# Performance work log

Hardware: AMD Instinct MI355X
Metric: run time of the kernel (lower is better)

## Reference

```python
import jax, jax.numpy as jnp
import numpy as np

B, C, H, W = 32, 2, 224, 224
P = 4096   # mask points per instance
N = 256    # HV_NUM_OF_HYPOTHESES


def setup_inputs() -> dict:
    key = jax.random.key(0)
    k1, k2, k3 = jax.random.split(key, 3)
    uv_img = jax.random.normal(k1, (B, C, H, W), dtype=jnp.float32)
    pts = jax.random.randint(k2, (B, P, 2), 0, H, dtype=jnp.int64 if jax.config.read('jax_enable_x64') else jnp.int32)
    pair_idx = jax.random.randint(k3, (B, N, 2), 0, P, dtype=pts.dtype)
    return {"uv_img": uv_img, "pts": pts, "pair_idx": pair_idx}


def _per_instance(uv, p, pi):
    # uv: [2,H,W], p: [P,2] int, pi: [N,2] int
    pt0 = p[pi[:, 0]]                      # [N,2] (row, col)
    pt1 = p[pi[:, 1]]                      # [N,2]
    # uv values at each sampled point: uv_img[:, row, col] -> [N,2]
    uv0 = uv[:, pt0[:, 0], pt0[:, 1]].T    # [N,2]
    uv1 = uv[:, pt1[:, 0], pt1[:, 1]].T    # [N,2]
    pt0f = pt0.astype(uv.dtype)
    pt1f = pt1.astype(uv.dtype)
    # A = [uv0 | -uv1], B = pt1 - pt0 (2x2 pinverse solve per hypothesis)
    A = jnp.stack([uv0, -uv1], axis=-1)    # [N,2,2]
    Bv = (pt1f - pt0f)[..., None]          # [N,2,1]
    X = jnp.matmul(jnp.linalg.pinv(A), Bv) # [N,2,1]
    Y = X[:, 0, :] * uv0 + pt0f            # [N,2] hypotheses (row, col)
    # hypothesis weights: count of mask points whose uv direction agrees
    pts_uv = uv[:, p[:, 0], p[:, 1]].T     # [P,2]
    a = Y[:, None, :] - p[None, :, :].astype(uv.dtype)      # [N,P,2]
    a = a / jnp.linalg.norm(a, axis=-1, keepdims=True)
    agree = jnp.einsum('npk,pk->np', a, pts_uv) > 0          # [N,P]
    w = jnp.sum(agree, axis=-1).astype(uv.dtype)             # [N]
    weighted_mean = jnp.sum(Y * w[:, None], axis=0) / jnp.sum(w)
    return weighted_mean[::-1]             # pixel_xy = (col, row)


def reference(uv_img, pts, pair_idx):
    # filled_pixel_xy: [B, 2]
    return jax.vmap(_per_instance)(uv_img, pts, pair_idx)
```

## Files before the change

### kernel.cpp

```cpp
#include <hip/hip_runtime.h>
#include <hip/hip_fp16.h>

#define BATCH 32
#define CH    2
#define HH    224
#define WW    224
#define PP    4096
#define NN    256
#define SPLIT 16
#define NBLK  (BATCH * SPLIT)
#define TILE  (PP / SPLIT)
#define TILE2 (TILE / 2)

#define WS_Y_OFF    0
#define WS_SY_OFF   (64 * 1024)
#define WS_SX_OFF   (WS_SY_OFF + NBLK * 4)
#define WS_SW_OFF   (WS_SX_OFF + NBLK * 4)
#define WS_NEED     (WS_SW_OFF + NBLK * 4)

struct alignas(16) PtPack { __half2 u, v, nc, pad; };

__device__ inline float2 solve_pair(const float* __restrict__ uvb,
                                    const int* __restrict__ ptsb,
                                    const int* __restrict__ pairb, int n)
{
    const int2 pr = *(const int2*)(pairb + n * 2);
    const int2 p0 = *(const int2*)(ptsb + pr.x * 2);
    const int2 p1 = *(const int2*)(ptsb + pr.y * 2);
    const int y0 = p0.x, x0 = p0.y;
    const int y1 = p1.x, x1 = p1.y;

    const float u0a = uvb[y0 * WW + x0];
    const float u0b = uvb[HH * WW + y0 * WW + x0];
    const float u1a = uvb[y1 * WW + x1];
    const float u1b = uvb[HH * WW + y1 * WW + x1];

    const double a00 = (double)u0a, a01 = -(double)u1a;
    const double a10 = (double)u0b, a11 = -(double)u1b;
    const double b0 = (double)(y1 - y0), b1 = (double)(x1 - x0);
    const double det = a00 * a11 - a01 * a10;
    const double frob2 = a00 * a00 + a01 * a01 + a10 * a10 + a11 * a11;

    double t0;
    if (fabs(det) > 1e-12 * frob2) {
        t0 = (b0 * a11 - b1 * a01) / det;
    } else if (frob2 > 0.0) {
        t0 = (a00 * b0 + a10 * b1) / frob2;
    } else {
        t0 = 0.0;
    }
    return make_float2((float)(t0 * (double)u0a + (double)y0),
                       (float)(t0 * (double)u0b + (double)x0));
}

__global__ __launch_bounds__(64)
void hough_solve(const float* __restrict__ uv,
                 const int* __restrict__ pts,
                 const int* __restrict__ pair,
                 float2* __restrict__ yv)
{
    const int blk = blockIdx.x;
    const int b = blk >> 2;
    const int n = ((blk & 3) << 6) + threadIdx.x;
    const float* uvb = uv + (size_t)b * CH * HH * WW;
    yv[b * NN + n] = solve_pair(uvb, pts + b * PP * 2, pair + b * NN * 2, n);
}

__global__ __launch_bounds__(256, 4)
void hough_vote(const float* __restrict__ uv,
                const int* __restrict__ pts,
                const float2* __restrict__ yv,
                float* __restrict__ psy,
                float* __restrict__ psx,
                float* __restrict__ psw)
{
    const int blk = blockIdx.x;
    const int b = blk / SPLIT;
    const int s = blk % SPLIT;
    const int t = threadIdx.x;

    const float* uvb = uv + (size_t)b * CH * HH * WW;
    const int* ptsb = pts + b * PP * 2;

    __shared__ PtPack tile[TILE2];
    {
        const int p = s * TILE + t;
        const int2 pyx = *(const int2*)(ptsb + p * 2);
        const float u = uvb[pyx.x * WW + pyx.y];
        const float v = uvb[HH * WW + pyx.x * WW + pyx.y];
        const float c = (float)pyx.x * u + (float)pyx.y * v;
        __half* base = (__half*)&tile[t >> 1];
        const int e = t & 1;
        base[0 + e] = __float2half_rn(u);
        base[2 + e] = __float2half_rn(v);
        base[4 + e] = __float2half_rn(-c);
    }

    const float2 Yn = yv[b * NN + t];
    const float yy = Yn.x, yx = Yn.y;
    const float maxab = fmaxf(fabsf(yy), fabsf(yx));
    const float sc = (maxab > 1024.0f) ? (1024.0f / maxab) : 1.0f;
    const __half2 yy2 = __float2half2_rn(yy * sc);
    const __half2 yx2 = __float2half2_rn(yx * sc);
    const __half2 sc2 = __float2half2_rn(sc);

    __syncthreads();

    unsigned negs = 0u;
    #pragma unroll 16
    for (int j = 0; j < TILE2; ++j) {
        const PtPack q = tile[j];
        __half2 d = __hmul2(yy2, q.u);
        d = __hfma2(yx2, q.v, d);
        d = __hfma2(sc2, q.nc, d);
        unsigned ub;
        __builtin_memcpy(&ub, &d, 4);
        negs += (ub >> 15) & 0x00010001u;
    }
    const int cw = TILE - (int)(negs & 0xFFFFu) - (int)(negs >> 16);

    float wy = (float)cw * yy;
    float wx = (float)cw * yx;
    float ww = (float)cw;
    #pragma unroll
    for (int off = 32; off > 0; off >>= 1) {
        wy += __shfl_down(wy, off);
        wx += __shfl_down(wx, off);
        ww += __shfl_down(ww, off);
    }

    __shared__ float red[4 * 3];
    const int wid = t >> 6;
    if ((t & 63) == 0) {
        red[wid * 3 + 0] = wy;
        red[wid * 3 + 1] = wx;
        red[wid * 3 + 2] = ww;
    }
    __syncthreads();
    if (t == 0) {
        psy[blk] = red[0] + red[3] + red[6] + red[9];
        psx[blk] = red[1] + red[4] + red[7] + red[10];
        psw[blk] = red[2] + red[5] + red[8] + red[11];
    }
}

__global__ __launch_bounds__(256)
void hough_final(const float* __restrict__ psy,
                 const float* __restrict__ psx,
                 const float* __restrict__ psw,
                 float* __restrict__ out)
{
    const int t = threadIdx.x;
    const int bb = t >> 3;
    const int l8 = t & 7;
    const int k = bb * SPLIT + l8 * 2;

    const float2 vy = *(const float2*)(psy + k);
    const float2 vx = *(const float2*)(psx + k);
    const float2 vw = *(const float2*)(psw + k);
    double sy = (double)vy.x + (double)vy.y;
    double sx = (double)vx.x + (double)vx.y;
    double sw = (double)vw.x + (double)vw.y;
    #pragma unroll
    for (int off = 1; off < 8; off <<= 1) {
        sy += __shfl_xor(sy, off);
        sx += __shfl_xor(sx, off);
        sw += __shfl_xor(sw, off);
    }
    if (l8 == 0) {
        out[bb * 2 + 0] = (float)(sx / sw);
        out[bb * 2 + 1] = (float)(sy / sw);
    }
}

__global__ __launch_bounds__(256, 4)
void hough_partial_fb(const float* __restrict__ uv,
                      const int* __restrict__ pts,
                      const int* __restrict__ pair,
                      float* __restrict__ psy,
                      float* __restrict__ psx,
                      float* __restrict__ psw)
{
    const int blk = blockIdx.x;
    const int b = blk / SPLIT;
    const int s = blk % SPLIT;
    const int t = threadIdx.x;

    const float* uvb = uv + (size_t)b * CH * HH * WW;
    const int* ptsb = pts + b * PP * 2;

    __shared__ PtPack tile[TILE2];
    {
        const int p = s * TILE + t;
        const int2 pyx = *(const int2*)(ptsb + p * 2);
        const float u = uvb[pyx.x * WW + pyx.y];
        const float v = uvb[HH * WW + pyx.x * WW + pyx.y];
        const float c = (float)pyx.x * u + (float)pyx.y * v;
        __half* base = (__half*)&tile[t >> 1];
        const int e = t & 1;
        base[0 + e] = __float2half_rn(u);
        base[2 + e] = __float2half_rn(v);
        base[4 + e] = __float2half_rn(-c);
    }

    const float2 Yn = solve_pair(uvb, ptsb, pair + b * NN * 2, t);
    const float yy = Yn.x, yx = Yn.y;
    const float maxab = fmaxf(fabsf(yy), fabsf(yx));
    const float sc = (maxab > 1024.0f) ? (1024.0f / maxab) : 1.0f;
    const __half2 yy2 = __float2half2_rn(yy * sc);
    const __half2 yx2 = __float2half2_rn(yx * sc);
    const __half2 sc2 = __float2half2_rn(sc);

    __syncthreads();

    unsigned negs = 0u;
    #pragma unroll 16
    for (int j = 0; j < TILE2; ++j) {
        const PtPack q = tile[j];
        __half2 d = __hmul2(yy2, q.u);
        d = __hfma2(yx2, q.v, d);
        d = __hfma2(sc2, q.nc, d);
        unsigned ub;
        __builtin_memcpy(&ub, &d, 4);
        negs += (ub >> 15) & 0x00010001u;
    }
    const int cw = TILE - (int)(negs & 0xFFFFu) - (int)(negs >> 16);

    float wy = (float)cw * yy;
    float wx = (float)cw * yx;
    float ww = (float)cw;
    #pragma unroll
    for (int off = 32; off > 0; off >>= 1) {
        wy += __shfl_down(wy, off);
        wx += __shfl_down(wx, off);
        ww += __shfl_down(ww, off);
    }
    __shared__ float red[4 * 3];
    const int wid = t >> 6;
    if ((t & 63) == 0) {
        red[wid * 3 + 0] = wy;
        red[wid * 3 + 1] = wx;
        red[wid * 3 + 2] = ww;
    }
    __syncthreads();
    if (t == 0) {
        psy[blk] = red[0] + red[3] + red[6] + red[9];
        psx[blk] = red[1] + red[4] + red[7] + red[10];
        psw[blk] = red[2] + red[5] + red[8] + red[11];
    }
}

extern "C" void kernel_launch(void* const* d_in, const int* in_sizes, int n_in,
                              void* d_out, int out_size, void* d_ws, size_t ws_size,
                              hipStream_t stream)
{
    const float* uv   = (const float*)d_in[0];
    const int*   pts  = (const int*)d_in[1];
    const int*   pair = (const int*)d_in[2];
    float* out = (float*)d_out;
    char* ws = (char*)d_ws;

    float* psy = (float*)(ws + WS_SY_OFF);
    float* psx = (float*)(ws + WS_SX_OFF);
    float* psw = (float*)(ws + WS_SW_OFF);

    if (ws_size >= WS_NEED) {
        float2* yv = (float2*)(ws + WS_Y_OFF);
        hough_solve<<<128, 64, 0, stream>>>(uv, pts, pair, yv);
        hough_vote<<<NBLK, 256, 0, stream>>>(uv, pts, yv, psy, psx, psw);
        hough_final<<<1, 256, 0, stream>>>(psy, psx, psw, out);
    } else {
        psy = (float*)ws; psx = psy + NBLK; psw = psx + NBLK;
        hough_partial_fb<<<NBLK, 256, 0, stream>>>(uv, pts, pair, psy, psx, psw);
        hough_final<<<1, 256, 0, stream>>>(psy, psx, psw, out);
    }
}
```

Before: 19.44 us.

## Split point tile across waves and give each lane four hypotheses

Each wave now handles a quarter of the shared point tile, and each lane evaluates four hypotheses (lane + 64*g) against every point it loads. One shared-memory load of a point pack then feeds four hypothesis dot products instead of one, cutting LDS traffic per FLOP by four. Per-lane counts are weighted before the wave reduction, so the totals stay the same. The cost is higher register pressure from holding four sets of hypothesis constants and four counters.

```diff
diff --git a/kernel.cpp b/kernel.cpp
--- a/kernel.cpp
+++ b/kernel.cpp
@@ -11,6 +11,7 @@
 #define NBLK  (BATCH * SPLIT)
 #define TILE  (PP / SPLIT)
 #define TILE2 (TILE / 2)
+#define WPACKS (TILE2 / 4)
 
 #define WS_Y_OFF    0
 #define WS_SY_OFF   (64 * 1024)
@@ -78,6 +79,8 @@
     const int b = blk / SPLIT;
     const int s = blk % SPLIT;
     const int t = threadIdx.x;
+    const int wave = t >> 6;
+    const int lane = t & 63;
 
     const float* uvb = uv + (size_t)b * CH * HH * WW;
     const int* ptsb = pts + b * PP * 2;
@@ -96,32 +99,51 @@
         base[4 + e] = __float2half_rn(-c);
     }
 
-    const float2 Yn = yv[b * NN + t];
-    const float yy = Yn.x, yx = Yn.y;
-    const float maxab = fmaxf(fabsf(yy), fabsf(yx));
-    const float sc = (maxab > 1024.0f) ? (1024.0f / maxab) : 1.0f;
-    const __half2 yy2 = __float2half2_rn(yy * sc);
-    const __half2 yx2 = __float2half2_rn(yx * sc);
-    const __half2 sc2 = __float2half2_rn(sc);
-
-    __syncthreads();
-
-    unsigned negs = 0u;
-    #pragma unroll 16
-    for (int j = 0; j < TILE2; ++j) {
-        const PtPack q = tile[j];
-        __half2 d = __hmul2(yy2, q.u);
-        d = __hfma2(yx2, q.v, d);
-        d = __hfma2(sc2, q.nc, d);
+    float yyf[4], yxf[4];
+    __half2 yy2[4], yx2[4], sc2[4];
+    #pragma unroll
+    for (int g = 0; g < 4; ++g) {
+        const float2 Yn = yv[b * NN + lane + 64 * g];
+        yyf[g] = Yn.x;
+        yxf[g] = Yn.y;
+        const float maxab = fmaxf(fabsf(Yn.x), fabsf(Yn.y));
+        const float sc = (maxab > 1024.0f) ? (1024.0f / maxab) : 1.0f;
+        yy2[g] = __float2half2_rn(Yn.x * sc);
+        yx2[g] = __float2half2_rn(Yn.y * sc);
+        sc2[g] = __float2half2_rn(sc);
+    }
+
+    __syncthreads();
+
+    unsigned negs0 = 0u, negs1 = 0u, negs2 = 0u, negs3 = 0u;
+    const PtPack* wp = tile + wave * WPACKS;
+    #pragma unroll 8
+    for (int j = 0; j < WPACKS; ++j) {
+        const PtPack q = wp[j];
         unsigned ub;
-        __builtin_memcpy(&ub, &d, 4);
-        negs += (ub >> 15) & 0x00010001u;
-    }
-    const int cw = TILE - (int)(negs & 0xFFFFu) - (int)(negs >> 16);
-
-    float wy = (float)cw * yy;
-    float wx = (float)cw * yx;
-    float ww = (float)cw;
+        __half2 d;
+        d = __hmul2(yy2[0], q.u); d = __hfma2(yx2[0], q.v, d); d = __hfma2(sc2[0], q.nc, d);
+        __builtin_memcpy(&ub, &d, 4); negs0 += (ub >> 15) & 0x00010001u;
+        d = __hmul2(yy2[1], q.u); d = __hfma2(yx2[1], q.v, d); d = __hfma2(sc2[1], q.nc, d);
+        __builtin_memcpy(&ub, &d, 4); negs1 += (ub >> 15) & 0x00010001u;
+        d = __hmul2(yy2[2], q.u); d = __hfma2(yx2[2], q.v, d); d = __hfma2(sc2[2], q.nc, d);
+        __builtin_memcpy(&ub, &d, 4); negs2 += (ub >> 15) & 0x00010001u;
+        d = __hmul2(yy2[3], q.u); d = __hfma2(yx2[3], q.v, d); d = __hfma2(sc2[3], q.nc, d);
+        __builtin_memcpy(&ub, &d, 4); negs3 += (ub >> 15) & 0x00010001u;
+    }
+
+    const int pts_per_lane = 2 * WPACKS;
+    const int c0 = pts_per_lane - (int)(negs0 & 0xFFFFu) - (int)(negs0 >> 16);
+    const int c1 = pts_per_lane - (int)(negs1 & 0xFFFFu) - (int)(negs1 >> 16);
+    const int c2 = pts_per_lane - (int)(negs2 & 0xFFFFu) - (int)(negs2 >> 16);
+    const int c3 = pts_per_lane - (int)(negs3 & 0xFFFFu) - (int)(negs3 >> 16);
+
+    float wy = (float)c0 * yyf[0] + (float)c1 * yyf[1]
+             + (float)c2 * yyf[2] + (float)c3 * yyf[3];
+    float wx = (float)c0 * yxf[0] + (float)c1 * yxf[1]
+             + (float)c2 * yxf[2] + (float)c3 * yxf[3];
+    float ww = (float)(c0 + c1 + c2 + c3);
+
     #pragma unroll
     for (int off = 32; off > 0; off >>= 1) {
         wy += __shfl_down(wy, off);
@@ -130,11 +152,10 @@
     }
 
     __shared__ float red[4 * 3];
-    const int wid = t >> 6;
-    if ((t & 63) == 0) {
-        red[wid * 3 + 0] = wy;
-        red[wid * 3 + 1] = wx;
-        red[wid * 3 + 2] = ww;
+    if (lane == 0) {
+        red[wave * 3 + 0] = wy;
+        red[wave * 3 + 1] = wx;
+        red[wave * 3 + 2] = ww;
     }
     __syncthreads();
     if (t == 0) {
```

After: 18.33 us. 5.7% less time.
